# Kernel optimization log

Hardware: AMD Instinct MI355X
Metric: run time of the kernel (lower is better)

## Reference

```python
import jax, jax.numpy as jnp
import numpy as np

L, D, HQ, HKV, HD, P, V, B, S = 4, 2048, 16, 4, 128, 8192, 32000, 2, 1024
THETA, EPS = 500000.0, 1e-5
RATIO = HQ // HKV  # GQA q-to-kv ratio = 4


def rmsnorm(x, w):
    # torch: w * (x * rsqrt(mean(x^2, -1) + eps)) computed in fp32
    x32 = x.astype(jnp.float32)
    n = x32 * jax.lax.rsqrt(jnp.mean(x32 * x32, axis=-1, keepdims=True) + EPS)
    return w * n.astype(x.dtype)


def make_rope(seq_len):
    inv = 1.0 / (THETA ** (jnp.arange(0, HD, 2, dtype=jnp.float32) / HD))  # [HD/2]
    ang = jnp.arange(seq_len, dtype=jnp.float32)[:, None] * inv[None, :]   # [S, HD/2]
    return jnp.cos(ang)[None, :, None, :], jnp.sin(ang)[None, :, None, :]  # [1,S,1,HD/2]


def rope(t, cos, sin):
    # torch code: complex = t[..., :HD/2] + i*t[..., HD/2:], multiply by e^{i*ang},
    # then view_as_real + flatten -> INTERLEAVED (r0,i0,r1,i1,...) output layout.
    h = HD // 2
    r, im = t[..., :h], t[..., h:]
    orr = r * cos - im * sin
    oim = r * sin + im * cos
    return jnp.stack([orr, oim], axis=-1).reshape(t.shape)


def attention(x, wqkv, wo, cos, sin):
    b, s, _ = x.shape
    qkv = x @ wqkv                               # [b,s,D+2*HKV*HD]
    q = qkv[..., :D].reshape(b, s, HQ, HD)
    k = qkv[..., D:D + HKV * HD].reshape(b, s, HKV, HD)
    v = qkv[..., D + HKV * HD:].reshape(b, s, HKV, HD)
    q = rope(q, cos, sin)
    k = rope(k, cos, sin)
    # GQA: repeat_interleave kv heads to match q heads (offset=0 prefill; cache is identity)
    k = jnp.repeat(k, RATIO, axis=2)
    v = jnp.repeat(v, RATIO, axis=2)
    scale = 1.0 / np.sqrt(HD)
    scores = jnp.einsum('bqhd,bkhd->bhqk', q, k) * scale
    causal = jnp.tril(jnp.ones((s, s), dtype=bool))
    scores = jnp.where(causal[None, None], scores, jnp.finfo(scores.dtype).min)
    probs = jax.nn.softmax(scores, axis=-1)
    out = jnp.einsum('bhqk,bkhd->bqhd', probs, v).reshape(b, s, D)
    return out @ wo


def swiglu(x, wgu, wd):
    gu = x @ wgu                                  # [b,s,2P]
    gate, up = gu[..., :P], gu[..., P:]
    return (jax.nn.silu(gate) * up) @ wd


def setup_inputs() -> dict:
    key = jax.random.key(0)
    ks = jax.random.split(key, 8)
    sc = 0.02
    return {
        'tokens': jax.random.randint(ks[0], (B, S), 0, V),
        'emb': jax.random.normal(ks[1], (V, D), jnp.float32) * sc,
        'w_qkv': jax.random.normal(ks[2], (L, D, D + 2 * HKV * HD), jnp.float32) * sc,
        'w_o': jax.random.normal(ks[3], (L, D, D), jnp.float32) * sc,
        'w_gate_up': jax.random.normal(ks[4], (L, D, 2 * P), jnp.float32) * sc,
        'w_down': jax.random.normal(ks[5], (L, P, D), jnp.float32) * sc,
        'ln_attn': jnp.ones((L, D), jnp.float32),
        'ln_ffn': jnp.ones((L, D), jnp.float32),
        'ln_f': jnp.ones((D,), jnp.float32),
        'w_lm': jax.random.normal(ks[6], (D, V), jnp.float32) * sc,
    }


def reference(tokens, emb, w_qkv, w_o, w_gate_up, w_down, ln_attn, ln_ffn, ln_f, w_lm):
    cos, sin = make_rope(S)
    x = emb[tokens]                               # [B,S,D]
    for l in range(L):
        x = x + attention(rmsnorm(x, ln_attn[l]), w_qkv[l], w_o[l], cos, sin)
        x = x + swiglu(rmsnorm(x, ln_ffn[l]), w_gate_up[l], w_down[l])
    return rmsnorm(x, ln_f) @ w_lm                # logits [B,S,V]
```

## Files before the change

kernel.cpp:

```cpp
#include <hip/hip_runtime.h>
#include <hip/hip_bf16.h>
#include <math.h>

#define S_LEN 1024
#define DIM   2048
#define NHQ   16
#define NHKV  4
#define HDIM  128
#define PDIM  8192
#define VOCAB 32000
#define NLAYER 4
#define NROWS (2 * S_LEN)

typedef __attribute__((ext_vector_type(4))) float f32x4;
typedef __attribute__((ext_vector_type(8))) short bf16x8;

__device__ __forceinline__ void gload_lds16(const void* g, void* l) {
  __builtin_amdgcn_global_load_lds(
      (const __attribute__((address_space(1))) unsigned int*)g,
      (__attribute__((address_space(3))) unsigned int*)l, 16, 0, 0);
}

#define FENCE() asm volatile("" ::: "memory")

__global__ __launch_bounds__(256) void k_embed(const int* __restrict__ tokens,
    const float* __restrict__ emb, float* __restrict__ x) {
  int row = blockIdx.x;
  int tok = tokens[row];
  const f32x4* src = (const f32x4*)(emb + (size_t)tok * DIM);
  f32x4* dst = (f32x4*)(x + (size_t)row * DIM);
  for (int i = threadIdx.x; i < DIM / 4; i += 256) dst[i] = src[i];
}

__global__ __launch_bounds__(256) void k_rmsnorm(const float* __restrict__ x,
    const float* __restrict__ w, __hip_bfloat16* __restrict__ out) {
  int row = blockIdx.x;
  const float* xr = x + (size_t)row * DIM;
  float ss = 0.f;
  for (int i = threadIdx.x; i < DIM; i += 256) { float v = xr[i]; ss += v * v; }
  for (int off = 32; off; off >>= 1) ss += __shfl_xor(ss, off);
  __shared__ float wsum[4];
  if ((threadIdx.x & 63) == 0) wsum[threadIdx.x >> 6] = ss;
  __syncthreads();
  float tot = wsum[0] + wsum[1] + wsum[2] + wsum[3];
  float r = rsqrtf(tot / (float)DIM + 1e-5f);
  __hip_bfloat16* orow = out + (size_t)row * DIM;
  for (int i = threadIdx.x; i < DIM; i += 256)
    orow[i] = __float2bfloat16(w[i] * (xr[i] * r));
}

__global__ __launch_bounds__(256) void k_wt(const float* __restrict__ W,
    __hip_bfloat16* __restrict__ WT, int K, int N) {
  __shared__ __hip_bfloat16 t[64][72];
  int k0 = blockIdx.y * 64, n0 = blockIdx.x * 64;
  int r = threadIdx.x >> 4;
  int c4 = (threadIdx.x & 15) * 4;
#pragma unroll
  for (int i = 0; i < 4; ++i) {
    int k = r + i * 16;
    f32x4 v = *(const f32x4*)(W + (size_t)(k0 + k) * N + n0 + c4);
#pragma unroll
    for (int j = 0; j < 4; ++j) t[c4 + j][k] = __float2bfloat16(v[j]);
  }
  __syncthreads();
  int n = threadIdx.x >> 2, kc = (threadIdx.x & 3) * 16;
  bf16x8* dst = (bf16x8*)(WT + (size_t)(n0 + n) * K + k0 + kc);
  dst[0] = *(const bf16x8*)&t[n][kc];
  dst[1] = *(const bf16x8*)&t[n][kc + 8];
}

__global__ __launch_bounds__(256) void k_wt_gu(const float* __restrict__ W,
    __hip_bfloat16* __restrict__ WT, int K, int N) {
  __shared__ __hip_bfloat16 t[64][72];
  int k0 = blockIdx.y * 64, n0 = blockIdx.x * 64;
  int r = threadIdx.x >> 4;
  int c4 = (threadIdx.x & 15) * 4;
  int nblk = (n0 + c4) >> 4;
  int jj   = (n0 + c4) & 15;
  int srcc = ((nblk & 1) ? PDIM : 0) + ((nblk >> 1) << 4) + jj;
#pragma unroll
  for (int i = 0; i < 4; ++i) {
    int k = r + i * 16;
    f32x4 v = *(const f32x4*)(W + (size_t)(k0 + k) * N + srcc);
#pragma unroll
    for (int j = 0; j < 4; ++j) t[c4 + j][k] = __float2bfloat16(v[j]);
  }
  __syncthreads();
  int n = threadIdx.x >> 2, kc = (threadIdx.x & 3) * 16;
  bf16x8* dst = (bf16x8*)(WT + (size_t)(n0 + n) * K + k0 + kc);
  dst[0] = *(const bf16x8*)&t[n][kc];
  dst[1] = *(const bf16x8*)&t[n][kc + 8];
}

template<int EPI>
__global__ __launch_bounds__(512) void k_gemm256(
    const __hip_bfloat16* __restrict__ A, const __hip_bfloat16* __restrict__ BT,
    void* __restrict__ Cv, int M, int N, int K) {
  __shared__ __hip_bfloat16 AsH[4][128][64];
  __shared__ __hip_bfloat16 BsH[4][128][64];
  const int NH = K >> 5;
  int tid = threadIdx.x;
  int bid = blockIdx.x;
  int mt = bid & 7, nt = bid >> 3;
  int bm = mt << 8, bn = nt << 8;
  int wave = tid >> 6, lane = tid & 63;
  int wm = wave >> 2, wn = wave & 3;
  int g = lane >> 4, c = lane & 15;
  f32x4 acc[8][4] = {};

  int pre  = (lane & 7) ^ (lane >> 3);
  int rOff = (lane >> 3) * 2 + (pre >> 2);
  int cOff = (pre & 3) * 8;

  auto stageA = [&](int S, int h) {
#pragma unroll
    for (int rd = 0; rd < 2; ++rd) {
      int seg = rd * 8 + wave;
      gload_lds16(A + (size_t)(bm + seg * 16 + rOff) * K + h * 32 + cOff,
                  &AsH[S][seg * 8 + (lane >> 3)][(lane & 7) * 8]);
    }
  };
  auto stageB = [&](int S, int h) {
#pragma unroll
    for (int rd = 0; rd < 2; ++rd) {
      int seg = rd * 8 + wave;
      gload_lds16(BT + (size_t)(bn + seg * 16 + rOff) * K + h * 32 + cOff,
                  &BsH[S][seg * 8 + (lane >> 3)][(lane & 7) * 8]);
    }
  };

  stageA(0, 0); stageB(0, 0);
  stageA(1, 1); stageB(1, 1);
  stageA(2, 2);
  asm volatile("s_waitcnt vmcnt(6)" ::: "memory");
  __builtin_amdgcn_s_barrier();
  FENCE();

  int lineA = wm * 64 + (c >> 1);
  int lineB = wn * 32 + (c >> 1);
  int slotE = ((((c & 1) << 2) | g) ^ (c >> 1)) * 8;

  for (int H = 0; H < NH; ++H) {
    int S = H & 3;
    bf16x8 af[8], bv[4];
#pragma unroll
    for (int mi = 0; mi < 8; ++mi)
      af[mi] = *(const bf16x8*)&AsH[S][lineA + mi * 8][slotE];
#pragma unroll
    for (int ni = 0; ni < 4; ++ni)
      bv[ni] = *(const bf16x8*)&BsH[S][lineB + ni * 8][slotE];
    FENCE();
    if (H + 2 < NH) stageB((H + 2) & 3, H + 2);
    if (H + 3 < NH) stageA((H + 3) & 3, H + 3);
    if (H + 4 <= NH)      { asm volatile("s_waitcnt vmcnt(6)" ::: "memory"); }
    else if (H + 3 == NH) { asm volatile("s_waitcnt vmcnt(4)" ::: "memory"); }
    else if (H + 2 == NH) { asm volatile("s_waitcnt vmcnt(0)" ::: "memory"); }
    __builtin_amdgcn_s_barrier();
    asm volatile("s_waitcnt lgkmcnt(0)" ::: "memory");
    __builtin_amdgcn_sched_barrier(0);
    __builtin_amdgcn_s_setprio(1);
#pragma unroll
    for (int mi = 0; mi < 8; ++mi)
#pragma unroll
      for (int ni = 0; ni < 4; ++ni)
        acc[mi][ni] = __builtin_amdgcn_mfma_f32_16x16x32_bf16(af[mi], bv[ni], acc[mi][ni], 0, 0, 0);
    __builtin_amdgcn_s_setprio(0);
    FENCE();
    __builtin_amdgcn_s_barrier();
    FENCE();
  }

  float* Cf = (float*)Cv;
  __hip_bfloat16* Cb = (__hip_bfloat16*)Cv;
  int row0 = bm + wm * 128, col0 = bn + wn * 64;
  if (EPI == 3) {
#pragma unroll
    for (int mi = 0; mi < 8; ++mi)
#pragma unroll
      for (int ni = 0; ni < 4; ni += 2)
#pragma unroll
        for (int r = 0; r < 4; ++r) {
          int row = row0 + mi * 16 + g * 4 + r;
          int hcol = ((col0 + ni * 16) >> 1) + c;
          float gate = acc[mi][ni][r], up = acc[mi][ni + 1][r];
          float sv = gate / (1.f + __expf(-gate)) * up;
          Cb[(size_t)row * PDIM + hcol] = __float2bfloat16(sv);
        }
  } else {
#pragma unroll
    for (int mi = 0; mi < 8; ++mi)
#pragma unroll
      for (int ni = 0; ni < 4; ++ni)
#pragma unroll
        for (int r = 0; r < 4; ++r) {
          int row = row0 + mi * 16 + g * 4 + r;
          int col = col0 + ni * 16 + c;
          size_t idx = (size_t)row * N + col;
          if (EPI == 0) Cf[idx] = acc[mi][ni][r];
          else if (EPI == 1) Cf[idx] += acc[mi][ni][r];
          else Cb[idx] = __float2bfloat16(acc[mi][ni][r]);
        }
  }
}

template<int EPI>
__global__ __launch_bounds__(256) void k_gemm_bt(
    const __hip_bfloat16* __restrict__ A, const __hip_bfloat16* __restrict__ BT,
    void* __restrict__ Cv, int M, int N, int K) {
  __shared__ __hip_bfloat16 As[2][128][64];
  __shared__ __hip_bfloat16 Bs[2][128][64];
  int nm = M >> 7;
  int bid = blockIdx.x;
  int mt, nt;
  if (nm == 16) {
    int xcd = bid & 7;
    int seq = bid >> 3;
    mt = (xcd << 1) | (seq & 1);
    nt = seq >> 1;
  } else {
    mt = bid % nm;
    nt = bid / nm;
  }
  int bm = mt << 7, bn = nt << 7;
  int tid  = threadIdx.x;
  int wave = tid >> 6, lane = tid & 63;
  int wr = (wave >> 1) * 64, wc = (wave & 1) * 64;
  int g = lane >> 4, c = lane & 15;
  f32x4 acc[4][4] = {};

  auto stage = [&](int buf, int k0) {
#pragma unroll
    for (int i = 0; i < 4; ++i) {
      int ci = i * 256 + tid;
      int row = ci >> 3, pc = ci & 7;
      int jl = pc ^ (row & 7);
      gload_lds16(A + (size_t)(bm + row) * K + k0 + jl * 8, &As[buf][row][pc * 8]);
      gload_lds16(BT + (size_t)(bn + row) * K + k0 + jl * 8, &Bs[buf][row][pc * 8]);
    }
  };

  int ntiles = K >> 6;
  stage(0, 0);
  if (ntiles > 1) stage(1, 64);

  for (int t = 0; t < ntiles; ++t) {
    int cur = t & 1;
    if (t + 1 < ntiles) asm volatile("s_waitcnt vmcnt(8)" ::: "memory");
    else                asm volatile("s_waitcnt vmcnt(0)" ::: "memory");
    __builtin_amdgcn_s_barrier();
    FENCE();
    __builtin_amdgcn_sched_barrier(0);
#pragma unroll
    for (int kk = 0; kk < 2; ++kk) {
      bf16x8 af[4], bv[4];
#pragma unroll
      for (int mi = 0; mi < 4; ++mi) {
        int row = wr + mi * 16 + c;
        int ch = (kk * 4 + g) ^ (row & 7);
        af[mi] = *(const bf16x8*)&As[cur][row][ch * 8];
      }
#pragma unroll
      for (int ni = 0; ni < 4; ++ni) {
        int row = wc + ni * 16 + c;
        int ch = (kk * 4 + g) ^ (row & 7);
        bv[ni] = *(const bf16x8*)&Bs[cur][row][ch * 8];
      }
      __builtin_amdgcn_s_setprio(1);
#pragma unroll
      for (int mi = 0; mi < 4; ++mi)
#pragma unroll
        for (int ni = 0; ni < 4; ++ni)
          acc[mi][ni] = __builtin_amdgcn_mfma_f32_16x16x32_bf16(af[mi], bv[ni], acc[mi][ni], 0, 0, 0);
      __builtin_amdgcn_s_setprio(0);
    }
    FENCE();
    __builtin_amdgcn_s_barrier();
    FENCE();
    if (t + 2 < ntiles) stage(cur, (t + 2) << 6);
  }

  float* Cf = (float*)Cv;
  __hip_bfloat16* Cb = (__hip_bfloat16*)Cv;
#pragma unroll
  for (int mi = 0; mi < 4; ++mi)
#pragma unroll
    for (int ni = 0; ni < 4; ++ni)
#pragma unroll
      for (int r = 0; r < 4; ++r) {
        int row = bm + wr + mi * 16 + g * 4 + r;
        int col = bn + wc + ni * 16 + c;
        size_t idx = (size_t)row * N + col;
        if (EPI == 0) Cf[idx] = acc[mi][ni][r];
        else if (EPI == 1) Cf[idx] += acc[mi][ni][r];
        else Cb[idx] = __float2bfloat16(acc[mi][ni][r]);
      }
}

template<int EPI>
__global__ __launch_bounds__(256) void k_gemm(
    const __hip_bfloat16* __restrict__ A, const float* __restrict__ Bw,
    void* __restrict__ Cv, int M, int N, int K) {
  __shared__ __hip_bfloat16 As[128][32];
  __shared__ __hip_bfloat16 Bs[128][40];
  int tid  = threadIdx.x;
  int bm = blockIdx.y * 128, bn = blockIdx.x * 128;
  int wave = tid >> 6, lane = tid & 63;
  int wr = (wave >> 1) * 64, wc = (wave & 1) * 64;
  int lrow = lane & 15, lk = (lane >> 4) * 8;
  f32x4 acc[4][4] = {};
  for (int k0 = 0; k0 < K; k0 += 32) {
#pragma unroll
    for (int i = 0; i < 2; ++i) {
      int L = i * 256 + tid;
      int row = L >> 2, koff = (L & 3) * 8;
      gload_lds16(A + (size_t)(bm + row) * K + k0 + koff, &As[row][koff]);
    }
#pragma unroll
    for (int i = 0; i < 4; ++i) {
      int L = i * 256 + tid;
      int kk = L >> 5;
      int c4 = (L & 31) * 4;
      f32x4 v = *(const f32x4*)(Bw + (size_t)(k0 + kk) * N + bn + c4);
#pragma unroll
      for (int j = 0; j < 4; ++j) Bs[c4 + j][kk] = __float2bfloat16(v[j]);
    }
    __syncthreads();
    bf16x8 af[4], bfr[4];
#pragma unroll
    for (int mi = 0; mi < 4; ++mi)
      af[mi] = *(const bf16x8*)(&As[wr + mi * 16 + lrow][lk]);
#pragma unroll
    for (int ni = 0; ni < 4; ++ni)
      bfr[ni] = *(const bf16x8*)(&Bs[wc + ni * 16 + lrow][lk]);
#pragma unroll
    for (int mi = 0; mi < 4; ++mi)
#pragma unroll
      for (int ni = 0; ni < 4; ++ni)
        acc[mi][ni] = __builtin_amdgcn_mfma_f32_16x16x32_bf16(af[mi], bfr[ni], acc[mi][ni], 0, 0, 0);
    __syncthreads();
  }
  float* Cf = (float*)Cv;
  __hip_bfloat16* Cb = (__hip_bfloat16*)Cv;
#pragma unroll
  for (int mi = 0; mi < 4; ++mi)
#pragma unroll
    for (int ni = 0; ni < 4; ++ni)
#pragma unroll
      for (int r = 0; r < 4; ++r) {
        int row = bm + wr + mi * 16 + ((lane >> 4) * 4 + r);
        int col = bn + wc + ni * 16 + (lane & 15);
        size_t idx = (size_t)row * N + col;
        if (EPI == 0) Cf[idx] = acc[mi][ni][r];
        else if (EPI == 1) Cf[idx] += acc[mi][ni][r];
        else Cb[idx] = __float2bfloat16(acc[mi][ni][r]);
      }
}

__global__ __launch_bounds__(256) void k_rope(const float* __restrict__ qkv,
    __hip_bfloat16* __restrict__ qr, __hip_bfloat16* __restrict__ kr,
    __hip_bfloat16* __restrict__ vt) {
  int rowid = blockIdx.x;
  int b = rowid >> 10, s = rowid & (S_LEN - 1);
  const float* src = qkv + (size_t)rowid * 3072;
  const float kInvLog = 0.20503692777f;
  const float scale = 0.08838834764831845f;
  __shared__ float cs[64], sn[64];
  if (threadIdx.x < 64) {
    float inv = expf(-(float)threadIdx.x * kInvLog);
    float a = (float)s * inv;
    sincosf(a, &sn[threadIdx.x], &cs[threadIdx.x]);
  }
  __syncthreads();
  for (int it = threadIdx.x; it < NHQ * 64; it += 256) {
    int h = it >> 6, i = it & 63;
    float re = src[h * HDIM + i], im = src[h * HDIM + 64 + i];
    size_t dst = ((size_t)(b * NHQ + h) * S_LEN + s) * HDIM;
    qr[dst + 2 * i]     = __float2bfloat16((re * cs[i] - im * sn[i]) * scale);
    qr[dst + 2 * i + 1] = __float2bfloat16((re * sn[i] + im * cs[i]) * scale);
  }
  for (int it = threadIdx.x; it < NHKV * 64; it += 256) {
    int h = it >> 6, i = it & 63;
    float re = src[DIM + h * HDIM + i], im = src[DIM + h * HDIM + 64 + i];
    size_t dst = ((size_t)(b * NHKV + h) * S_LEN + s) * HDIM;
    kr[dst + 2 * i]     = __float2bfloat16(re * cs[i] - im * sn[i]);
    kr[dst + 2 * i + 1] = __float2bfloat16(re * sn[i] + im * cs[i]);
  }
  for (int it = threadIdx.x; it < NHKV * HDIM; it += 256) {
    int h = it >> 7, d = it & 127;
    vt[(((size_t)b * NHKV + h) * HDIM + d) * S_LEN + s] =
        __float2bfloat16(src[DIM + NHKV * HDIM + it]);
  }
}

__global__ __launch_bounds__(256) void k_attn_mfma(
    const __hip_bfloat16* __restrict__ Q,
    const __hip_bfloat16* __restrict__ Kc,
    const __hip_bfloat16* __restrict__ VT,
    __hip_bfloat16* __restrict__ O) {
  __shared__ __hip_bfloat16 plds[4][16][40];
  int wave = threadIdx.x >> 6, lane = threadIdx.x & 63;
  int gw = blockIdx.x * 4 + wave;
  int qt = gw & 63;
  int bh = gw >> 6;
  int b = bh >> 4, h = bh & 15;
  int hk = h >> 2;
  int q0 = qt * 16;
  int g = lane >> 4, c = lane & 15;
  const __hip_bfloat16* Qb = Q + ((size_t)bh * S_LEN + q0) * HDIM;
  const __hip_bfloat16* Kb = Kc + (size_t)(b * NHKV + hk) * S_LEN * HDIM;
  const __hip_bfloat16* Vb = VT + (size_t)(b * NHKV + hk) * S_LEN * HDIM;

  bf16x8 qf[4];
#pragma unroll
  for (int cn = 0; cn < 4; ++cn)
    qf[cn] = *(const bf16x8*)(Qb + (size_t)c * HDIM + cn * 32 + g * 8);

  f32x4 po[8] = {};
  float m[4], l[4];
#pragma unroll
  for (int r = 0; r < 4; ++r) { m[r] = -1e30f; l[r] = 0.f; }

  int kvend = q0 + 16;
  for (int kv0 = 0; kv0 < kvend; kv0 += 32) {
    f32x4 s0 = {}, s1 = {};
#pragma unroll
    for (int cn = 0; cn < 4; ++cn) {
      bf16x8 k0f = *(const bf16x8*)(Kb + (size_t)(kv0 + c) * HDIM + cn * 32 + g * 8);
      bf16x8 k1f = *(const bf16x8*)(Kb + (size_t)(kv0 + 16 + c) * HDIM + cn * 32 + g * 8);
      s0 = __builtin_amdgcn_mfma_f32_16x16x32_bf16(qf[cn], k0f, s0, 0, 0, 0);
      s1 = __builtin_amdgcn_mfma_f32_16x16x32_bf16(qf[cn], k1f, s1, 0, 0, 0);
    }
    if (kv0 + 31 > q0) {
#pragma unroll
      for (int r = 0; r < 4; ++r) {
        int qrow = q0 + g * 4 + r;
        if (kv0 + c > qrow)      s0[r] = -1e30f;
        if (kv0 + 16 + c > qrow) s1[r] = -1e30f;
      }
    }
    float rm[4];
#pragma unroll
    for (int r = 0; r < 4; ++r) rm[r] = fmaxf(s0[r], s1[r]);
#pragma unroll
    for (int off = 1; off < 16; off <<= 1)
#pragma unroll
      for (int r = 0; r < 4; ++r) rm[r] = fmaxf(rm[r], __shfl_xor(rm[r], off));
    float p0[4], p1[4], rs[4];
#pragma unroll
    for (int r = 0; r < 4; ++r) {
      float mn = fmaxf(m[r], rm[r]);
      float corr = __expf(m[r] - mn);
      m[r] = mn;
      p0[r] = __expf(s0[r] - mn);
      p1[r] = __expf(s1[r] - mn);
      rs[r] = p0[r] + p1[r];
      l[r] *= corr;
#pragma unroll
      for (int t = 0; t < 8; ++t) po[t][r] *= corr;
    }
#pragma unroll
    for (int off = 1; off < 16; off <<= 1)
#pragma unroll
      for (int r = 0; r < 4; ++r) rs[r] += __shfl_xor(rs[r], off);
#pragma unroll
    for (int r = 0; r < 4; ++r) l[r] += rs[r];
#pragma unroll
    for (int r = 0; r < 4; ++r) {
      plds[wave][g * 4 + r][c]      = __float2bfloat16(p0[r]);
      plds[wave][g * 4 + r][16 + c] = __float2bfloat16(p1[r]);
    }
    bf16x8 pf = *(const bf16x8*)&plds[wave][c][g * 8];
#pragma unroll
    for (int t = 0; t < 8; ++t) {
      bf16x8 vf = *(const bf16x8*)(Vb + (size_t)(t * 16 + c) * S_LEN + kv0 + g * 8);
      po[t] = __builtin_amdgcn_mfma_f32_16x16x32_bf16(pf, vf, po[t], 0, 0, 0);
    }
  }
  float inv[4];
#pragma unroll
  for (int r = 0; r < 4; ++r) inv[r] = 1.f / l[r];
  __hip_bfloat16* ob = O + ((size_t)(b * S_LEN) + q0) * DIM + h * HDIM;
#pragma unroll
  for (int t = 0; t < 8; ++t)
#pragma unroll
    for (int r = 0; r < 4; ++r)
      ob[(size_t)(g * 4 + r) * DIM + t * 16 + c] = __float2bfloat16(po[t][r] * inv[r]);
}

extern "C" void kernel_launch(void* const* d_in, const int* in_sizes, int n_in,
                              void* d_out, int out_size, void* d_ws, size_t ws_size,
                              hipStream_t stream) {
  const int*   tokens    = (const int*)d_in[0];
  const float* emb       = (const float*)d_in[1];
  const float* w_qkv     = (const float*)d_in[2];
  const float* w_o       = (const float*)d_in[3];
  const float* w_gate_up = (const float*)d_in[4];
  const float* w_down    = (const float*)d_in[5];
  const float* ln_attn   = (const float*)d_in[6];
  const float* ln_ffn    = (const float*)d_in[7];
  const float* ln_f      = (const float*)d_in[8];
  const float* w_lm      = (const float*)d_in[9];
  float* out = (float*)d_out;

  char* ws = (char*)d_ws;
  float* x = (float*)ws;                    ws += (size_t)NROWS * DIM * 4;
  __hip_bfloat16* xn = (__hip_bfloat16*)ws; ws += (size_t)NROWS * DIM * 2;
  float* qkv = (float*)ws;                  ws += (size_t)NROWS * 3072 * 4;
  __hip_bfloat16* qr = (__hip_bfloat16*)ws; ws += (size_t)2 * NHQ * S_LEN * HDIM * 2;
  __hip_bfloat16* kr = (__hip_bfloat16*)ws; ws += (size_t)2 * NHKV * S_LEN * HDIM * 2;
  __hip_bfloat16* vt = (__hip_bfloat16*)ws; ws += (size_t)2 * NHKV * S_LEN * HDIM * 2;
  __hip_bfloat16* ao = (__hip_bfloat16*)ws; ws += (size_t)NROWS * DIM * 2;
  __hip_bfloat16* gu = (__hip_bfloat16*)ws; ws += (size_t)NROWS * 2 * PDIM * 2;
  __hip_bfloat16* hb = (__hip_bfloat16*)ws; ws += (size_t)NROWS * PDIM * 2;
  __hip_bfloat16* wbuf = (__hip_bfloat16*)ws;
  size_t need = (size_t)(ws - (char*)d_ws) + (size_t)VOCAB * DIM * 2;
  bool bf16w = ws_size >= need;
  (void)gu;

  k_embed<<<NROWS, 256, 0, stream>>>(tokens, emb, x);

  for (int l = 0; l < NLAYER; ++l) {
    k_rmsnorm<<<NROWS, 256, 0, stream>>>(x, ln_attn + (size_t)l * DIM, xn);
    if (bf16w) {
      k_wt<<<dim3(3072 / 64, DIM / 64), 256, 0, stream>>>(
          w_qkv + (size_t)l * DIM * 3072, wbuf, DIM, 3072);
      k_gemm_bt<0><<<(NROWS / 128) * (3072 / 128), 256, 0, stream>>>(
          xn, wbuf, qkv, NROWS, 3072, DIM);
    } else {
      k_gemm<0><<<dim3(3072 / 128, NROWS / 128), 256, 0, stream>>>(
          xn, w_qkv + (size_t)l * DIM * 3072, qkv, NROWS, 3072, DIM);
    }
    k_rope<<<NROWS, 256, 0, stream>>>(qkv, qr, kr, vt);
    k_attn_mfma<<<(2 * NHQ * (S_LEN / 16)) / 4, 256, 0, stream>>>(qr, kr, vt, ao);
    if (bf16w) {
      k_wt<<<dim3(DIM / 64, DIM / 64), 256, 0, stream>>>(
          w_o + (size_t)l * DIM * DIM, wbuf, DIM, DIM);
      k_gemm_bt<1><<<(NROWS / 128) * (DIM / 128), 256, 0, stream>>>(
          ao, wbuf, x, NROWS, DIM, DIM);
    } else {
      k_gemm<1><<<dim3(DIM / 128, NROWS / 128), 256, 0, stream>>>(
          ao, w_o + (size_t)l * DIM * DIM, x, NROWS, DIM, DIM);
    }
    k_rmsnorm<<<NROWS, 256, 0, stream>>>(x, ln_ffn + (size_t)l * DIM, xn);
    if (bf16w) {
      k_wt_gu<<<dim3(2 * PDIM / 64, DIM / 64), 256, 0, stream>>>(
          w_gate_up + (size_t)l * DIM * 2 * PDIM, wbuf, DIM, 2 * PDIM);
      k_gemm256<3><<<8 * (2 * PDIM / 256), 512, 0, stream>>>(
          xn, wbuf, hb, NROWS, 2 * PDIM, DIM);
    } else {
      k_gemm<2><<<dim3(2 * PDIM / 128, NROWS / 128), 256, 0, stream>>>(
          xn, w_gate_up + (size_t)l * DIM * 2 * PDIM, (void*)hb, NROWS, 2 * PDIM, DIM);
    }
    if (bf16w) {
      k_wt<<<dim3(DIM / 64, PDIM / 64), 256, 0, stream>>>(
          w_down + (size_t)l * PDIM * DIM, wbuf, PDIM, DIM);
      k_gemm_bt<1><<<(NROWS / 128) * (DIM / 128), 256, 0, stream>>>(
          hb, wbuf, x, NROWS, DIM, PDIM);
    } else {
      k_gemm<1><<<dim3(DIM / 128, NROWS / 128), 256, 0, stream>>>(
          hb, w_down + (size_t)l * PDIM * DIM, x, NROWS, DIM, PDIM);
    }
  }

  k_rmsnorm<<<NROWS, 256, 0, stream>>>(x, ln_f, xn);
  if (bf16w) {
    k_wt<<<dim3(VOCAB / 64, DIM / 64), 256, 0, stream>>>(w_lm, wbuf, DIM, VOCAB);
    k_gemm256<0><<<8 * (VOCAB / 256), 512, 0, stream>>>(
        xn, wbuf, out, NROWS, VOCAB, DIM);
  } else {
    k_gemm<0><<<dim3(VOCAB / 128, NROWS / 128), 256, 0, stream>>>(
        xn, w_lm, out, NROWS, VOCAB, DIM);
  }
}
```

Baseline: 2.618 ms.

## Split-K atomics for residual GEMMs, bf16 QKV output, reorder gemm256 prefetch

The o-proj and down-proj residual GEMMs now use a split-K of 2 and accumulate into x with atomicAdd. This doubles the block count (256 to 512 tiles) so more of the GPU is filled. The QKV projection writes bf16 instead of fp32, which halves that buffer's write and read traffic in the rope kernel at some precision cost. The gemm256 pipeline now prefetches A two stages ahead and B three stages ahead instead of the reverse. The atomics make the accumulation order non-deterministic and add read-modify-write traffic on x.

```diff
diff --git a/kernel.cpp b/kernel.cpp
--- a/kernel.cpp
+++ b/kernel.cpp
@@ -131,7 +131,7 @@
 
   stageA(0, 0); stageB(0, 0);
   stageA(1, 1); stageB(1, 1);
-  stageA(2, 2);
+  stageB(2, 2);
   asm volatile("s_waitcnt vmcnt(6)" ::: "memory");
   __builtin_amdgcn_s_barrier();
   FENCE();
@@ -150,8 +150,8 @@
     for (int ni = 0; ni < 4; ++ni)
       bv[ni] = *(const bf16x8*)&BsH[S][lineB + ni * 8][slotE];
     FENCE();
-    if (H + 2 < NH) stageB((H + 2) & 3, H + 2);
-    if (H + 3 < NH) stageA((H + 3) & 3, H + 3);
+    if (H + 2 < NH) stageA((H + 2) & 3, H + 2);
+    if (H + 3 < NH) stageB((H + 3) & 3, H + 3);
     if (H + 4 <= NH)      { asm volatile("s_waitcnt vmcnt(6)" ::: "memory"); }
     else if (H + 3 == NH) { asm volatile("s_waitcnt vmcnt(4)" ::: "memory"); }
     else if (H + 2 == NH) { asm volatile("s_waitcnt vmcnt(0)" ::: "memory"); }
@@ -203,7 +203,7 @@
   }
 }
 
-template<int EPI>
+template<int EPI, int KSPLIT = 1>
 __global__ __launch_bounds__(256) void k_gemm_bt(
     const __hip_bfloat16* __restrict__ A, const __hip_bfloat16* __restrict__ BT,
     void* __restrict__ Cv, int M, int N, int K) {
@@ -222,6 +222,8 @@
     nt = bid / nm;
   }
   int bm = mt << 7, bn = nt << 7;
+  const int Keff = K / KSPLIT;
+  const int kbase = (KSPLIT > 1) ? (int)blockIdx.y * Keff : 0;
   int tid  = threadIdx.x;
   int wave = tid >> 6, lane = tid & 63;
   int wr = (wave >> 1) * 64, wc = (wave & 1) * 64;
@@ -234,12 +236,12 @@
       int ci = i * 256 + tid;
       int row = ci >> 3, pc = ci & 7;
       int jl = pc ^ (row & 7);
-      gload_lds16(A + (size_t)(bm + row) * K + k0 + jl * 8, &As[buf][row][pc * 8]);
-      gload_lds16(BT + (size_t)(bn + row) * K + k0 + jl * 8, &Bs[buf][row][pc * 8]);
+      gload_lds16(A + (size_t)(bm + row) * K + kbase + k0 + jl * 8, &As[buf][row][pc * 8]);
+      gload_lds16(BT + (size_t)(bn + row) * K + kbase + k0 + jl * 8, &Bs[buf][row][pc * 8]);
     }
   };
 
-  int ntiles = K >> 6;
+  int ntiles = Keff >> 6;
   stage(0, 0);
   if (ntiles > 1) stage(1, 64);
 
@@ -292,7 +294,8 @@
         size_t idx = (size_t)row * N + col;
         if (EPI == 0) Cf[idx] = acc[mi][ni][r];
         else if (EPI == 1) Cf[idx] += acc[mi][ni][r];
-        else Cb[idx] = __float2bfloat16(acc[mi][ni][r]);
+        else if (EPI == 2) Cb[idx] = __float2bfloat16(acc[mi][ni][r]);
+        else atomicAdd(&Cf[idx], acc[mi][ni][r]);
       }
 }
 
@@ -356,12 +359,12 @@
       }
 }
 
-__global__ __launch_bounds__(256) void k_rope(const float* __restrict__ qkv,
+__global__ __launch_bounds__(256) void k_rope(const __hip_bfloat16* __restrict__ qkv,
     __hip_bfloat16* __restrict__ qr, __hip_bfloat16* __restrict__ kr,
     __hip_bfloat16* __restrict__ vt) {
   int rowid = blockIdx.x;
   int b = rowid >> 10, s = rowid & (S_LEN - 1);
-  const float* src = qkv + (size_t)rowid * 3072;
+  const __hip_bfloat16* src = qkv + (size_t)rowid * 3072;
   const float kInvLog = 0.20503692777f;
   const float scale = 0.08838834764831845f;
   __shared__ float cs[64], sn[64];
@@ -373,22 +376,23 @@
   __syncthreads();
   for (int it = threadIdx.x; it < NHQ * 64; it += 256) {
     int h = it >> 6, i = it & 63;
-    float re = src[h * HDIM + i], im = src[h * HDIM + 64 + i];
+    float re = __bfloat162float(src[h * HDIM + i]);
+    float im = __bfloat162float(src[h * HDIM + 64 + i]);
     size_t dst = ((size_t)(b * NHQ + h) * S_LEN + s) * HDIM;
     qr[dst + 2 * i]     = __float2bfloat16((re * cs[i] - im * sn[i]) * scale);
     qr[dst + 2 * i + 1] = __float2bfloat16((re * sn[i] + im * cs[i]) * scale);
   }
   for (int it = threadIdx.x; it < NHKV * 64; it += 256) {
     int h = it >> 6, i = it & 63;
-    float re = src[DIM + h * HDIM + i], im = src[DIM + h * HDIM + 64 + i];
+    float re = __bfloat162float(src[DIM + h * HDIM + i]);
+    float im = __bfloat162float(src[DIM + h * HDIM + 64 + i]);
     size_t dst = ((size_t)(b * NHKV + h) * S_LEN + s) * HDIM;
     kr[dst + 2 * i]     = __float2bfloat16(re * cs[i] - im * sn[i]);
     kr[dst + 2 * i + 1] = __float2bfloat16(re * sn[i] + im * cs[i]);
   }
   for (int it = threadIdx.x; it < NHKV * HDIM; it += 256) {
     int h = it >> 7, d = it & 127;
-    vt[(((size_t)b * NHKV + h) * HDIM + d) * S_LEN + s] =
-        __float2bfloat16(src[DIM + NHKV * HDIM + it]);
+    vt[(((size_t)b * NHKV + h) * HDIM + d) * S_LEN + s] = src[DIM + NHKV * HDIM + it];
   }
 }
 
@@ -505,17 +509,15 @@
   char* ws = (char*)d_ws;
   float* x = (float*)ws;                    ws += (size_t)NROWS * DIM * 4;
   __hip_bfloat16* xn = (__hip_bfloat16*)ws; ws += (size_t)NROWS * DIM * 2;
-  float* qkv = (float*)ws;                  ws += (size_t)NROWS * 3072 * 4;
+  __hip_bfloat16* qkvb = (__hip_bfloat16*)ws; ws += (size_t)NROWS * 3072 * 2;
   __hip_bfloat16* qr = (__hip_bfloat16*)ws; ws += (size_t)2 * NHQ * S_LEN * HDIM * 2;
   __hip_bfloat16* kr = (__hip_bfloat16*)ws; ws += (size_t)2 * NHKV * S_LEN * HDIM * 2;
   __hip_bfloat16* vt = (__hip_bfloat16*)ws; ws += (size_t)2 * NHKV * S_LEN * HDIM * 2;
   __hip_bfloat16* ao = (__hip_bfloat16*)ws; ws += (size_t)NROWS * DIM * 2;
-  __hip_bfloat16* gu = (__hip_bfloat16*)ws; ws += (size_t)NROWS * 2 * PDIM * 2;
   __hip_bfloat16* hb = (__hip_bfloat16*)ws; ws += (size_t)NROWS * PDIM * 2;
   __hip_bfloat16* wbuf = (__hip_bfloat16*)ws;
   size_t need = (size_t)(ws - (char*)d_ws) + (size_t)VOCAB * DIM * 2;
   bool bf16w = ws_size >= need;
-  (void)gu;
 
   k_embed<<<NROWS, 256, 0, stream>>>(tokens, emb, x);
 
@@ -524,18 +526,18 @@
     if (bf16w) {
       k_wt<<<dim3(3072 / 64, DIM / 64), 256, 0, stream>>>(
           w_qkv + (size_t)l * DIM * 3072, wbuf, DIM, 3072);
-      k_gemm_bt<0><<<(NROWS / 128) * (3072 / 128), 256, 0, stream>>>(
-          xn, wbuf, qkv, NROWS, 3072, DIM);
+      k_gemm_bt<2><<<(NROWS / 128) * (3072 / 128), 256, 0, stream>>>(
+          xn, wbuf, qkvb, NROWS, 3072, DIM);
     } else {
-      k_gemm<0><<<dim3(3072 / 128, NROWS / 128), 256, 0, stream>>>(
-          xn, w_qkv + (size_t)l * DIM * 3072, qkv, NROWS, 3072, DIM);
-    }
-    k_rope<<<NROWS, 256, 0, stream>>>(qkv, qr, kr, vt);
+      k_gemm<2><<<dim3(3072 / 128, NROWS / 128), 256, 0, stream>>>(
+          xn, w_qkv + (size_t)l * DIM * 3072, qkvb, NROWS, 3072, DIM);
+    }
+    k_rope<<<NROWS, 256, 0, stream>>>(qkvb, qr, kr, vt);
     k_attn_mfma<<<(2 * NHQ * (S_LEN / 16)) / 4, 256, 0, stream>>>(qr, kr, vt, ao);
     if (bf16w) {
       k_wt<<<dim3(DIM / 64, DIM / 64), 256, 0, stream>>>(
           w_o + (size_t)l * DIM * DIM, wbuf, DIM, DIM);
-      k_gemm_bt<1><<<(NROWS / 128) * (DIM / 128), 256, 0, stream>>>(
+      k_gemm_bt<4, 2><<<dim3((NROWS / 128) * (DIM / 128), 2), 256, 0, stream>>>(
           ao, wbuf, x, NROWS, DIM, DIM);
     } else {
       k_gemm<1><<<dim3(DIM / 128, NROWS / 128), 256, 0, stream>>>(
@@ -554,7 +556,7 @@
     if (bf16w) {
       k_wt<<<dim3(DIM / 64, PDIM / 64), 256, 0, stream>>>(
           w_down + (size_t)l * PDIM * DIM, wbuf, PDIM, DIM);
-      k_gemm_bt<1><<<(NROWS / 128) * (DIM / 128), 256, 0, stream>>>(
+      k_gemm_bt<4, 2><<<dim3((NROWS / 128) * (DIM / 128), 2), 256, 0, stream>>>(
           hb, wbuf, x, NROWS, DIM, PDIM);
     } else {
       k_gemm<1><<<dim3(DIM / 128, NROWS / 128), 256, 0, stream>>>(
```

New measurement: 2.425 ms. -7.3%, faster.
